# Kernel tuning notes

Hardware: AMD Instinct MI355X
Metric: run time of the kernel (lower is better)

## Reference

```python
import jax, jax.numpy as jnp
import numpy as np

B, T, C, HS = 8, 2048, 768, 256  # batch, seq(block_size), n_embed, head_size


def setup_inputs() -> dict:
    key = jax.random.key(0)
    kx, kq, kk, kv = jax.random.split(key, 4)
    scale = 1.0 / np.sqrt(C)
    return {
        "x": jax.random.normal(kx, (B, T, C), dtype=jnp.float32),
        # torch nn.Linear(n_embed, head_size, bias=False) computes x @ W.T;
        # store weights pre-transposed as [in, out].
        "Wq": jax.random.normal(kq, (C, HS), dtype=jnp.float32) * scale,
        "Wk": jax.random.normal(kk, (C, HS), dtype=jnp.float32) * scale,
        "Wv": jax.random.normal(kv, (C, HS), dtype=jnp.float32) * scale,
    }


def reference(x, Wq, Wk, Wv):
    Bx, Tx, Cx = x.shape
    q = x @ Wq  # [B,T,HS]
    k = x @ Wk  # [B,T,HS]
    v = x @ Wv  # [B,T,HS]
    # NOTE: original scales by C**-0.5 with C = n_embed (not head_size)
    att = jnp.einsum('btd,bsd->bts', q, k) * (Cx ** -0.5)  # [B,T,T]
    causal = jnp.tril(jnp.ones((Tx, Tx), dtype=bool))
    att = jnp.where(causal, att, -jnp.inf)
    probs = jax.nn.softmax(att, axis=-1)
    # dropout=0.0 -> identity (eval mode)
    out = jnp.einsum('bts,bsd->btd', probs, v)  # [B,T,HS]
    return out
```

## Files before the change

kernel.cpp:

```cpp
#include <hip/hip_runtime.h>
#include <hip/hip_bf16.h>
#include <math.h>

#define B_  8
#define T_  2048
#define C_  768
#define HS_ 256

#define CHUNKS_PER_BATCH 80
#define NSLOT (CHUNKS_PER_BATCH * B_)

typedef float  f32x4  __attribute__((ext_vector_type(4)));
typedef __bf16 bf16x8 __attribute__((ext_vector_type(8)));
typedef __bf16 bf16x4 __attribute__((ext_vector_type(4)));
typedef __bf16 bf16x2 __attribute__((ext_vector_type(2)));

#define MFMA16(a, b, c) __builtin_amdgcn_mfma_f32_16x16x32_bf16((a), (b), (c), 0, 0, 0)

#define GLOAD_LDS16(gp, lp)                                                     \
    __builtin_amdgcn_global_load_lds(                                           \
        (const __attribute__((address_space(1))) void*)(gp),                    \
        (__attribute__((address_space(3))) void*)(lp), 16, 0, 0)

__device__ __forceinline__ int chunk_cum64(int qb) {
    int g = qb >> 3;
    return 4 * g * (g + 1) + (qb & 7) * (g + 1);
}

__global__ __launch_bounds__(256) void prep_kernel(const float* __restrict__ x,
                                                   const float* __restrict__ Wq,
                                                   const float* __restrict__ Wk,
                                                   const float* __restrict__ Wv,
                                                   __bf16* __restrict__ xb,
                                                   __bf16* __restrict__ wt_all,
                                                   float qscale) {
    const int bid = blockIdx.x;
    if (bid < 6144) {
        size_t i = ((size_t)bid * 256 + threadIdx.x) * 8;
        f32x4 a = *(const f32x4*)(x + i);
        f32x4 b = *(const f32x4*)(x + i + 4);
        bf16x8 o;
        o[0] = (__bf16)a[0]; o[1] = (__bf16)a[1]; o[2] = (__bf16)a[2]; o[3] = (__bf16)a[3];
        o[4] = (__bf16)b[0]; o[5] = (__bf16)b[1]; o[6] = (__bf16)b[2]; o[7] = (__bf16)b[3];
        *(bf16x8*)(xb + i) = o;
    } else {
        int idx = (bid - 6144) * 256 + threadIdx.x;
        int n   = idx & 255;
        int t   = idx >> 8;
        int mat = t / 96;
        int k8  = t - mat * 96;
        const float* W = (mat == 0) ? Wq : ((mat == 1) ? Wk : Wv);
        float scale = (mat == 0) ? qscale : 1.0f;
        bf16x8 o;
#pragma unroll
        for (int j = 0; j < 8; j++)
            o[j] = (__bf16)(W[(k8 * 8 + j) * HS_ + n] * scale);
        *(bf16x8*)&wt_all[((size_t)mat * HS_ + n) * C_ + k8 * 8] = o;
    }
}

__global__ __launch_bounds__(256) void proj_kernel(const __bf16* __restrict__ xb,
                                                   const __bf16* __restrict__ wt,
                                                   __bf16* __restrict__ qf_,
                                                   __bf16* __restrict__ kf_,
                                                   __bf16* __restrict__ vf_) {
    __shared__ alignas(16) __bf16 ldsA[2][128 * 32];
    __shared__ alignas(16) __bf16 ldsB[2][128 * 32];

    const int tid  = threadIdx.x;
    const int w    = tid >> 6;
    const int lane = tid & 63;
    const int cm   = lane & 15;
    const int quad = lane >> 4;
    const int wm   = w & 1;
    const int wn   = w >> 1;
    const int m0   = blockIdx.x * 128;
    const int n0   = blockIdx.y * 128;
    const int mat  = n0 >> 8;

    f32x4 acc[4][4];
#pragma unroll
    for (int i = 0; i < 4; i++)
#pragma unroll
        for (int j = 0; j < 4; j++) acc[i][j] = (f32x4){0.f, 0.f, 0.f, 0.f};

#pragma unroll
    for (int h = 0; h < 2; h++) {
        int c = tid + h * 256;
        GLOAD_LDS16(xb + (size_t)(m0 + (c >> 2)) * C_ + (c & 3) * 8, &ldsA[0][c * 8]);
        GLOAD_LDS16(wt + (size_t)(n0 + (c >> 2)) * C_ + (c & 3) * 8, &ldsB[0][c * 8]);
    }

    for (int kt = 0; kt < 24; kt++) {
        const int cur = kt & 1;
        __syncthreads();

        if (kt < 23) {
            const int k0 = (kt + 1) * 32;
#pragma unroll
            for (int h = 0; h < 2; h++) {
                int c = tid + h * 256;
                GLOAD_LDS16(xb + (size_t)(m0 + (c >> 2)) * C_ + k0 + (c & 3) * 8,
                            &ldsA[cur ^ 1][c * 8]);
                GLOAD_LDS16(wt + (size_t)(n0 + (c >> 2)) * C_ + k0 + (c & 3) * 8,
                            &ldsB[cur ^ 1][c * 8]);
            }
        }

        bf16x8 af[4], bfr[4];
#pragma unroll
        for (int mt = 0; mt < 4; mt++)
            af[mt] = *(const bf16x8*)&ldsA[cur][(wm * 64 + mt * 16 + cm) * 32 + quad * 8];
#pragma unroll
        for (int nt = 0; nt < 4; nt++)
            bfr[nt] = *(const bf16x8*)&ldsB[cur][(wn * 64 + nt * 16 + cm) * 32 + quad * 8];
        if (mat < 2) {
#pragma unroll
            for (int dt = 0; dt < 4; dt++)
#pragma unroll
                for (int qt2 = 0; qt2 < 4; qt2++)
                    acc[dt][qt2] = MFMA16(bfr[dt], af[qt2], acc[dt][qt2]);
        } else {
#pragma unroll
            for (int mt = 0; mt < 4; mt++)
#pragma unroll
                for (int nt = 0; nt < 4; nt++)
                    acc[mt][nt] = MFMA16(af[mt], bfr[nt], acc[mt][nt]);
        }
    }

    const int dBase = (n0 & 255) + wn * 64;
    const int b     = m0 >> 11;
    if (mat < 2) {
        const int rt2 = ((m0 & 2047) >> 6) + wm;
        __bf16* dst = (mat == 0) ? qf_ : kf_;
#pragma unroll
        for (int dt = 0; dt < 4; dt++)
#pragma unroll
            for (int qt2 = 0; qt2 < 4; qt2++) {
                int d0    = dBase + dt * 16 + quad * 4;
                int ksq   = d0 >> 5;
                int quadp = (d0 >> 3) & 3;
                int j0    = d0 & 7;
                size_t addr;
                if (mat == 0)
                    addr = ((((size_t)(b * 32 + rt2) * 4 + qt2) * 8 + ksq) * 64
                            + quadp * 16 + cm) * 8 + j0;
                else
                    addr = ((((size_t)(b * 32 + rt2) * 8 + ksq) * 4 + qt2) * 64
                            + quadp * 16 + cm) * 8 + j0;
                bf16x4 v4;
                v4[0] = (__bf16)acc[dt][qt2][0]; v4[1] = (__bf16)acc[dt][qt2][1];
                v4[2] = (__bf16)acc[dt][qt2][2]; v4[3] = (__bf16)acc[dt][qt2][3];
                *(bf16x4*)(dst + addr) = v4;
            }
    } else {
        const int rt = ((m0 & 2047) + wm * 64) >> 6;
#pragma unroll
        for (int mt = 0; mt < 4; mt++) {
            int ks2   = (mt >> 1) & 1;
            int quadF = (mt & 1) * 2 + (quad >> 1);
            int jb    = (quad & 1) * 4;
#pragma unroll
            for (int nt = 0; nt < 4; nt++) {
                int ntv = (dBase >> 4) + nt;
                size_t idx = ((((size_t)(b * 32 + rt) * 2 + ks2) * 16 + ntv) * 64
                              + quadF * 16 + cm) * 8 + jb;
                bf16x4 v4;
                v4[0] = (__bf16)acc[mt][nt][0]; v4[1] = (__bf16)acc[mt][nt][1];
                v4[2] = (__bf16)acc[mt][nt][2]; v4[3] = (__bf16)acc[mt][nt][3];
                *(bf16x4*)(vf_ + idx) = v4;
            }
        }
    }
}

__global__ __launch_bounds__(256, 3) void flash_part(const __bf16* __restrict__ qf_,
                                                     const __bf16* __restrict__ kf_,
                                                     const __bf16* __restrict__ vf_,
                                                     __bf16* __restrict__ Opart,
                                                     float* __restrict__ mpart,
                                                     float* __restrict__ lpart) {
    __shared__ alignas(16) __bf16 ldsK[8 * 2 * 64 * 8];
    __shared__ alignas(16) __bf16 ldsV[16 * 64 * 8];
    __shared__ alignas(16) __bf16 ldsP[4][512];

    const int tid  = threadIdx.x;
    const int w    = tid >> 6;
    const int lane = tid & 63;
    const int cm   = lane & 15;
    const int quad = lane >> 4;

    const int pid  = blockIdx.x;
    const int b    = pid & 7;
    const int r    = (CHUNKS_PER_BATCH - 1) - (pid >> 3);
    int qb = 0, ci = 0;
    {
        int rr = r;
        for (int j = 0; j < 32; j++) {
            int c = (j >> 3) + 1;
            if (rr < c) { qb = j; ci = rr; break; }
            rr -= c;
        }
    }
    const int lpid = b * CHUNKS_PER_BATCH + r;
    const int kt_begin = ci * 16;
    const int kt_end   = min(kt_begin + 16, 2 * qb + 2);

    const __bf16* qp = qf_ + (((size_t)(b * 32 + qb) * 4 + w) * 8) * 512 + lane * 8;
    bf16x8 qf[8];
#pragma unroll
    for (int ks = 0; ks < 8; ks++) qf[ks] = *(const bf16x8*)(qp + ks * 512);

    f32x4 accO[16];
#pragma unroll
    for (int i = 0; i < 16; i++) accO[i] = (f32x4){0.f, 0.f, 0.f, 0.f};
    float mi = 0.f, li = 0.f;

    const int wrow  = qb * 64 + w * 16;
    const int qglob = wrow + cm;

    for (int kt = kt_begin; kt < kt_end; kt++) {
        __syncthreads();

        {
            const int kt64 = kt >> 1, kh = kt & 1;
            const __bf16* kgb = kf_ + (((size_t)(b * 32 + kt64) * 8) * 4 + kh * 2) * 512;
#pragma unroll
            for (int h = 0; h < 4; h++) {
                int g = h * 256 + tid;
                int ks = g >> 7, sub = g & 127;
                GLOAD_LDS16(kgb + (size_t)ks * 4 * 512 + sub * 8,
                            ldsK + (h * 256 + w * 64) * 8);
            }
            const __bf16* vgb = vf_ + ((size_t)(b * 64 + kt) * 16) * 512;
#pragma unroll
            for (int h = 0; h < 4; h++) {
                int g = h * 256 + tid;
                GLOAD_LDS16(vgb + (size_t)g * 8,
                            ldsV + (h * 256 + w * 64) * 8);
            }
        }
        __syncthreads();

        f32x4 s[2];
#pragma unroll
        for (int i = 0; i < 2; i++) s[i] = (f32x4){0.f, 0.f, 0.f, 0.f};
#pragma unroll
        for (int ns = 0; ns < 2; ns++)
#pragma unroll
            for (int ks = 0; ks < 8; ks++) {
                bf16x8 kfr = *(const bf16x8*)&ldsK[(ks * 2 + ns) * 512 + lane * 8];
                s[ns] = MFMA16(kfr, qf[ks], s[ns]);
            }
        if (kt * 32 + 31 > wrow) {
#pragma unroll
            for (int ns = 0; ns < 2; ns++)
#pragma unroll
                for (int i = 0; i < 4; i++)
                    if (kt * 32 + ns * 16 + quad * 4 + i > qglob)
                        s[ns][i] = -__builtin_inff();
        }
        if (kt == kt_begin) {
            float pm = -__builtin_inff();
#pragma unroll
            for (int ns = 0; ns < 2; ns++)
#pragma unroll
                for (int i = 0; i < 4; i++) pm = fmaxf(pm, s[ns][i]);
            pm = fmaxf(pm, __shfl_xor(pm, 16));
            pm = fmaxf(pm, __shfl_xor(pm, 32));
            mi = pm;
        }
        float p[2][4], rs = 0.f;
#pragma unroll
        for (int ns = 0; ns < 2; ns++)
#pragma unroll
            for (int i = 0; i < 4; i++) {
                p[ns][i] = exp2f(s[ns][i] - mi);
                rs += p[ns][i];
            }
        rs += __shfl_xor(rs, 16);
        rs += __shfl_xor(rs, 32);
        li += rs;

#pragma unroll
        for (int ns = 0; ns < 2; ns++)
#pragma unroll
            for (int i2 = 0; i2 < 2; i2++) {
                bf16x2 d2;
                d2[0] = (__bf16)p[ns][2 * i2];
                d2[1] = (__bf16)p[ns][2 * i2 + 1];
                int off = ((ns * 2 + (quad >> 1)) * 16 + cm) * 8
                          + (quad & 1) * 4 + i2 * 2;
                *(bf16x2*)&ldsP[w][off] = d2;
            }
        bf16x8 pfrag = *(const bf16x8*)&ldsP[w][(quad * 16 + cm) * 8];
#pragma unroll
        for (int nt = 0; nt < 16; nt++) {
            bf16x8 vfr = *(const bf16x8*)&ldsV[(nt * 64 + lane) * 8];
            accO[nt] = MFMA16(vfr, pfrag, accO[nt]);
        }
    }

    __bf16* op = Opart + ((size_t)lpid * 64 + w * 16 + cm) * HS_;
#pragma unroll
    for (int nt = 0; nt < 16; nt++) {
        bf16x4 v4;
        v4[0] = (__bf16)accO[nt][0]; v4[1] = (__bf16)accO[nt][1];
        v4[2] = (__bf16)accO[nt][2]; v4[3] = (__bf16)accO[nt][3];
        *(bf16x4*)(op + nt * 16 + quad * 4) = v4;
    }
    if (quad == 0) {
        mpart[lpid * 64 + w * 16 + cm] = mi;
        lpart[lpid * 64 + w * 16 + cm] = li;
    }
}

__global__ __launch_bounds__(256) void flash_combine(const __bf16* __restrict__ Opart,
                                                     const float* __restrict__ mpart,
                                                     const float* __restrict__ lpart,
                                                     float* __restrict__ out) {
    const int b    = blockIdx.x >> 5;
    const int qb   = blockIdx.x & 31;
    const int nc   = (qb >> 3) + 1;
    const int pid0 = b * CHUNKS_PER_BATCH + chunk_cum64(qb);

    const int tid  = threadIdx.x;
    const int col  = (tid & 63) * 4;
    const int r0   = blockIdx.y * 16 + (tid >> 6) * 4;

    f32x4 ms = (f32x4){-__builtin_inff(), -__builtin_inff(),
                       -__builtin_inff(), -__builtin_inff()};
    for (int c = 0; c < nc; c++) {
        f32x4 m4 = *(const f32x4*)(mpart + (pid0 + c) * 64 + r0);
#pragma unroll
        for (int i = 0; i < 4; i++) ms[i] = fmaxf(ms[i], m4[i]);
    }
    f32x4 acc[4];
#pragma unroll
    for (int i = 0; i < 4; i++) acc[i] = (f32x4){0.f, 0.f, 0.f, 0.f};
    f32x4 lt = (f32x4){0.f, 0.f, 0.f, 0.f};
    for (int c = 0; c < nc; c++) {
        f32x4 m4 = *(const f32x4*)(mpart + (pid0 + c) * 64 + r0);
        f32x4 l4 = *(const f32x4*)(lpart + (pid0 + c) * 64 + r0);
#pragma unroll
        for (int i = 0; i < 4; i++) {
            float sc = exp2f(m4[i] - ms[i]);
            lt[i] += l4[i] * sc;
            bf16x4 o = *(const bf16x4*)(Opart
                        + ((size_t)(pid0 + c) * 64 + r0 + i) * HS_ + col);
            acc[i][0] += (float)o[0] * sc; acc[i][1] += (float)o[1] * sc;
            acc[i][2] += (float)o[2] * sc; acc[i][3] += (float)o[3] * sc;
        }
    }
#pragma unroll
    for (int i = 0; i < 4; i++) {
        float inv = 1.0f / lt[i];
        f32x4 res = (f32x4){acc[i][0] * inv, acc[i][1] * inv,
                            acc[i][2] * inv, acc[i][3] * inv};
        *(f32x4*)(out + ((size_t)(b * T_ + qb * 64 + r0 + i)) * HS_ + col) = res;
    }
}

extern "C" void kernel_launch(void* const* d_in, const int* in_sizes, int n_in,
                              void* d_out, int out_size, void* d_ws, size_t ws_size,
                              hipStream_t stream) {
    const float* x  = (const float*)d_in[0];
    const float* Wq = (const float*)d_in[1];
    const float* Wk = (const float*)d_in[2];
    const float* Wv = (const float*)d_in[3];
    float* out = (float*)d_out;

    char* ws = (char*)d_ws;
    size_t off = 0;
    __bf16* wt_all = (__bf16*)(ws + off); off += 1179648;
    __bf16* qfrag  = (__bf16*)(ws + off); off += 8388608;
    __bf16* kfrag  = (__bf16*)(ws + off); off += 8388608;
    __bf16* vfrag  = (__bf16*)(ws + off); off += 8388608;
    __bf16* xb     = (__bf16*)(ws + off);
    __bf16* Opart  = (__bf16*)(ws + off); off += (size_t)NSLOT * 64 * HS_ * 2;
    float*  mpart  = (float*)(ws + off);  off += (size_t)NSLOT * 64 * 4;
    float*  lpart  = (float*)(ws + off);

    float qscale = 1.4426950408889634f / sqrtf((float)C_);

    prep_kernel<<<dim3(6432), 256, 0, stream>>>(x, Wq, Wk, Wv, xb, wt_all, qscale);
    proj_kernel<<<dim3(128, 6), 256, 0, stream>>>(xb, wt_all, qfrag, kfrag, vfrag);
    flash_part<<<dim3(NSLOT), 256, 0, stream>>>(qfrag, kfrag, vfrag, Opart, mpart, lpart);
    flash_combine<<<dim3(256, 4), 256, 0, stream>>>(Opart, mpart, lpart, out);
}
```

Before: 174.3 us.

## Double-buffer K/V tiles in LDS and split attention into smaller KV chunks

```diff
diff --git a/kernel.cpp b/kernel.cpp
--- a/kernel.cpp
+++ b/kernel.cpp
@@ -7,7 +7,7 @@
 #define C_  768
 #define HS_ 256
 
-#define CHUNKS_PER_BATCH 80
+#define CHUNKS_PER_BATCH 144
 #define NSLOT (CHUNKS_PER_BATCH * B_)
 
 typedef float  f32x4  __attribute__((ext_vector_type(4)));
@@ -23,8 +23,8 @@
         (__attribute__((address_space(3))) void*)(lp), 16, 0, 0)
 
 __device__ __forceinline__ int chunk_cum64(int qb) {
-    int g = qb >> 3;
-    return 4 * g * (g + 1) + (qb & 7) * (g + 1);
+    int g = qb >> 2;
+    return 2 * g * (g + 1) + (qb & 3) * (g + 1);
 }
 
 __global__ __launch_bounds__(256) void prep_kernel(const float* __restrict__ x,
@@ -175,14 +175,14 @@
     }
 }
 
-__global__ __launch_bounds__(256, 3) void flash_part(const __bf16* __restrict__ qf_,
+__global__ __launch_bounds__(256, 2) void flash_part(const __bf16* __restrict__ qf_,
                                                      const __bf16* __restrict__ kf_,
                                                      const __bf16* __restrict__ vf_,
                                                      __bf16* __restrict__ Opart,
                                                      float* __restrict__ mpart,
                                                      float* __restrict__ lpart) {
-    __shared__ alignas(16) __bf16 ldsK[8 * 2 * 64 * 8];
-    __shared__ alignas(16) __bf16 ldsV[16 * 64 * 8];
+    __shared__ alignas(16) __bf16 ldsK[2][8 * 2 * 64 * 8];
+    __shared__ alignas(16) __bf16 ldsV[2][16 * 64 * 8];
     __shared__ alignas(16) __bf16 ldsP[4][512];
 
     const int tid  = threadIdx.x;
@@ -198,20 +198,39 @@
     {
         int rr = r;
         for (int j = 0; j < 32; j++) {
-            int c = (j >> 3) + 1;
+            int c = (j >> 2) + 1;
             if (rr < c) { qb = j; ci = rr; break; }
             rr -= c;
         }
     }
     const int lpid = b * CHUNKS_PER_BATCH + r;
-    const int kt_begin = ci * 16;
-    const int kt_end   = min(kt_begin + 16, 2 * qb + 2);
+    const int kt_begin = ci * 8;
+    const int kt_end   = min(kt_begin + 8, 2 * qb + 2);
 
     const __bf16* qp = qf_ + (((size_t)(b * 32 + qb) * 4 + w) * 8) * 512 + lane * 8;
     bf16x8 qf[8];
 #pragma unroll
     for (int ks = 0; ks < 8; ks++) qf[ks] = *(const bf16x8*)(qp + ks * 512);
 
+    auto stage = [&](int bsel, int kt) {
+        const int kt64 = kt >> 1, kh = kt & 1;
+        const __bf16* kgb = kf_ + (((size_t)(b * 32 + kt64) * 8) * 4 + kh * 2) * 512;
+#pragma unroll
+        for (int h = 0; h < 4; h++) {
+            int g = h * 256 + tid;
+            int ks = g >> 7, sub = g & 127;
+            GLOAD_LDS16(kgb + (size_t)ks * 4 * 512 + sub * 8,
+                        &ldsK[bsel][(h * 256 + w * 64) * 8]);
+        }
+        const __bf16* vgb = vf_ + ((size_t)(b * 64 + kt) * 16) * 512;
+#pragma unroll
+        for (int h = 0; h < 4; h++) {
+            int g = h * 256 + tid;
+            GLOAD_LDS16(vgb + (size_t)g * 8,
+                        &ldsV[bsel][(h * 256 + w * 64) * 8]);
+        }
+    };
+
     f32x4 accO[16];
 #pragma unroll
     for (int i = 0; i < 16; i++) accO[i] = (f32x4){0.f, 0.f, 0.f, 0.f};
@@ -220,39 +239,26 @@
     const int wrow  = qb * 64 + w * 16;
     const int qglob = wrow + cm;
 
+    stage(0, kt_begin);
+    asm volatile("s_waitcnt vmcnt(0)" ::: "memory");
+    __builtin_amdgcn_s_barrier();
+
+    int cur = 0;
     for (int kt = kt_begin; kt < kt_end; kt++) {
-        __syncthreads();
-
-        {
-            const int kt64 = kt >> 1, kh = kt & 1;
-            const __bf16* kgb = kf_ + (((size_t)(b * 32 + kt64) * 8) * 4 + kh * 2) * 512;
-#pragma unroll
-            for (int h = 0; h < 4; h++) {
-                int g = h * 256 + tid;
-                int ks = g >> 7, sub = g & 127;
-                GLOAD_LDS16(kgb + (size_t)ks * 4 * 512 + sub * 8,
-                            ldsK + (h * 256 + w * 64) * 8);
-            }
-            const __bf16* vgb = vf_ + ((size_t)(b * 64 + kt) * 16) * 512;
-#pragma unroll
-            for (int h = 0; h < 4; h++) {
-                int g = h * 256 + tid;
-                GLOAD_LDS16(vgb + (size_t)g * 8,
-                            ldsV + (h * 256 + w * 64) * 8);
-            }
-        }
-        __syncthreads();
+        if (kt + 1 < kt_end) stage(cur ^ 1, kt + 1);
 
         f32x4 s[2];
 #pragma unroll
         for (int i = 0; i < 2; i++) s[i] = (f32x4){0.f, 0.f, 0.f, 0.f};
+        __builtin_amdgcn_s_setprio(1);
 #pragma unroll
         for (int ns = 0; ns < 2; ns++)
 #pragma unroll
             for (int ks = 0; ks < 8; ks++) {
-                bf16x8 kfr = *(const bf16x8*)&ldsK[(ks * 2 + ns) * 512 + lane * 8];
+                bf16x8 kfr = *(const bf16x8*)&ldsK[cur][(ks * 2 + ns) * 512 + lane * 8];
                 s[ns] = MFMA16(kfr, qf[ks], s[ns]);
             }
+        __builtin_amdgcn_s_setprio(0);
         if (kt * 32 + 31 > wrow) {
 #pragma unroll
             for (int ns = 0; ns < 2; ns++)
@@ -295,11 +301,17 @@
                 *(bf16x2*)&ldsP[w][off] = d2;
             }
         bf16x8 pfrag = *(const bf16x8*)&ldsP[w][(quad * 16 + cm) * 8];
+        __builtin_amdgcn_s_setprio(1);
 #pragma unroll
         for (int nt = 0; nt < 16; nt++) {
-            bf16x8 vfr = *(const bf16x8*)&ldsV[(nt * 64 + lane) * 8];
+            bf16x8 vfr = *(const bf16x8*)&ldsV[cur][(nt * 64 + lane) * 8];
             accO[nt] = MFMA16(vfr, pfrag, accO[nt]);
         }
+        __builtin_amdgcn_s_setprio(0);
+
+        asm volatile("s_waitcnt vmcnt(0)" ::: "memory");
+        __builtin_amdgcn_s_barrier();
+        cur ^= 1;
     }
 
     __bf16* op = Opart + ((size_t)lpid * 64 + w * 16 + cm) * HS_;
@@ -322,7 +334,7 @@
                                                      float* __restrict__ out) {
     const int b    = blockIdx.x >> 5;
     const int qb   = blockIdx.x & 31;
-    const int nc   = (qb >> 3) + 1;
+    const int nc   = (qb >> 2) + 1;
     const int pid0 = b * CHUNKS_PER_BATCH + chunk_cum64(qb);
 
     const int tid  = threadIdx.x;
```

Measured after the change: 184.6 us. +5.9%, slower.
